# Kernel optimization log

Hardware: AMD Instinct MI355X
Metric: run time of the kernel (lower is better)

Reference implementation:

```python
import jax, jax.numpy as jnp
import numpy as np

B, S, H, L, V = 32, 128, 1024, 2, 32000


def setup_inputs() -> dict:
    key = jax.random.key(0)
    ks = jax.random.split(key, 9)
    scale = 1.0 / np.sqrt(H)
    return {
        "x": jax.random.randint(ks[0], (B, 1), 0, V),
        "hidden": jax.random.normal(ks[1], (L, B, H), jnp.float32) * 0.1,
        "cell": jax.random.normal(ks[2], (L, B, H), jnp.float32) * 0.1,
        "target": jax.random.randint(ks[3], (B, S), 0, V),
        "tf_ratio": 1,  # teacher forcing always on -> deterministic
        "emb": jax.random.normal(ks[4], (V, H), jnp.float32) * 0.02,
        "w_ih": jax.random.normal(ks[5], (L, 4 * H, H), jnp.float32) * scale,
        "w_hh": jax.random.normal(ks[6], (L, 4 * H, H), jnp.float32) * scale,
        "b_ih": jax.random.normal(ks[7], (L, 4 * H), jnp.float32) * scale,
        "b_hh": jax.random.normal(ks[8], (L, 4 * H), jnp.float32) * scale,
    }


def _lstm_decode(tokens, h0, c0, emb, w_ih, w_hh, b_ih, b_hh):
    # tokens: [B,S] int; embed all teacher-forced inputs at once
    x_seq = emb[tokens]                      # [B,S,H]
    x_tbh = jnp.swapaxes(x_seq, 0, 1)        # [S,B,H]
    n_layers = h0.shape[0]

    def step(carry, x_t):
        h, c = carry                         # each [L,B,H]
        inp = x_t                            # [B,H]
        hs, cs = [], []
        for l in range(n_layers):
            # PyTorch gate order: i, f, g, o
            z = inp @ w_ih[l].T + h[l] @ w_hh[l].T + b_ih[l] + b_hh[l]
            i, f, g, o = jnp.split(z, 4, axis=-1)
            c_new = jax.nn.sigmoid(f) * c[l] + jax.nn.sigmoid(i) * jnp.tanh(g)
            h_new = jax.nn.sigmoid(o) * jnp.tanh(c_new)
            hs.append(h_new)
            cs.append(c_new)
            inp = h_new
        return (jnp.stack(hs), jnp.stack(cs)), inp

    _, outs = jax.lax.scan(step, (h0, c0), x_tbh)  # outs: [S,B,H]
    out = jnp.swapaxes(outs, 0, 1)                 # [B,S,H]
    # tied-weight projection to vocab
    return jnp.einsum("bsh,vh->bsv", out, emb)     # [B,S,V]


def reference(x, hidden, cell, target, tf_ratio, emb, w_ih, w_hh, b_ih, b_hh):
    # tf_ratio == 1: step 0 consumes x, step i>=1 consumes target[:, i]
    tokens = jnp.concatenate([x, target[:, 1:]], axis=1)  # [B,S]
    return _lstm_decode(tokens, hidden, cell, emb, w_ih, w_hh, b_ih, b_hh)
```

## Files before the change

kernel.cpp:

```cpp
#include <hip/hip_runtime.h>
#include <stdint.h>


typedef __attribute__((ext_vector_type(8))) short short8;
typedef __attribute__((ext_vector_type(4))) float f32x4;

#define MFMA16(a, b, c) __builtin_amdgcn_mfma_f32_16x16x32_bf16((a), (b), (c), 0, 0, 0)

__device__ __forceinline__ unsigned short f2bf(float f) {
  union { float f; unsigned int u; } v; v.f = f;
  unsigned int u = v.u;
  return (unsigned short)((u + 0x7fffu + ((u >> 16) & 1u)) >> 16);
}

__device__ __forceinline__ void gload_lds16(const unsigned short* g, unsigned short* l) {
  __builtin_amdgcn_global_load_lds(
      (const __attribute__((address_space(1))) void*)g,
      (__attribute__((address_space(3))) void*)l, 16, 0, 0);
}

__device__ __forceinline__ void st_u32_dev(unsigned* p, unsigned v) {
  __hip_atomic_store(p, v, __ATOMIC_RELAXED, __HIP_MEMORY_SCOPE_AGENT);
}
__device__ __forceinline__ unsigned ld_u32_dev(const unsigned* p) {
  return __hip_atomic_load(p, __ATOMIC_RELAXED, __HIP_MEMORY_SCOPE_AGENT);
}


__global__ void cvt_bf16_k(const float* __restrict__ s, unsigned short* __restrict__ d, int n4) {
  int i = blockIdx.x * blockDim.x + threadIdx.x;
  int st = gridDim.x * blockDim.x;
  for (; i < n4; i += st) {
    float4 v = ((const float4*)s)[i];
    ushort4 o;
    o.x = f2bf(v.x); o.y = f2bf(v.y); o.z = f2bf(v.z); o.w = f2bf(v.w);
    ((ushort4*)d)[i] = o;
  }
}

__global__ void init_small_k(const float* __restrict__ hidden,
                             const float* __restrict__ b_ih, const float* __restrict__ b_hh,
                             unsigned short* __restrict__ h0, unsigned short* __restrict__ h1,
                             float* __restrict__ bsum) {
  int bb = blockIdx.x;
  int tid = threadIdx.x;
  if (bb < 64) {
    const float* src = hidden + (bb < 32 ? 0 : 32768);
    unsigned short* dst = (bb < 32) ? h0 : h1;
    int i = (bb & 31) * 256 + tid;
    float4 v = ((const float4*)src)[i];
    ushort4 u;
    u.x = f2bf(v.x); u.y = f2bf(v.y); u.z = f2bf(v.z); u.w = f2bf(v.w);
    ((ushort4*)dst)[i] = u;
  } else {
    int i = (bb - 64) * 256 + tid;
    bsum[i] = b_ih[i] + b_hh[i];
  }
}

__global__ void embed_k(const int* __restrict__ x, const int* __restrict__ tgt,
                        const float* __restrict__ emb, unsigned short* __restrict__ xseq) {
  int row = blockIdx.x;
  int t = row >> 5, b = row & 31;
  int tok = (t == 0) ? x[b] : tgt[b * 128 + t];
  const float4* e = (const float4*)(emb + (size_t)tok * 1024);
  ushort4* o = (ushort4*)(xseq + (size_t)row * 1024);
  int i = threadIdx.x;
  float4 v = e[i];
  ushort4 u;
  u.x = f2bf(v.x); u.y = f2bf(v.y); u.z = f2bf(v.z); u.w = f2bf(v.w);
  o[i] = u;
}


__global__ __launch_bounds__(256, 2) void gemm_bf16_k(
    const unsigned short* __restrict__ A, const unsigned short* __restrict__ B,
    float* __restrict__ C, const float* __restrict__ bias, int N, int permC) {
  __shared__ __align__(16) unsigned short smem[32768];
  const int tid = threadIdx.x;
  const int lane = tid & 63;
  const int w = tid >> 6;
  const int wm = w >> 1, wn = w & 1;
  const int xcd = blockIdx.x & 7;
  const int idx = blockIdx.x >> 3;
  const int nBase = (idx >> 2) * 128;
  const int mBase = (xcd * 4 + (idx & 3)) * 128;
  const int lr = lane & 15, lk = lane >> 4;
  const int K = 1024;

  const int srow = tid >> 3;
  const int scol = (tid & 7) ^ (srow & 7);
  const int wchunk = tid & 192;

  f32x4 acc[4][4];
#pragma unroll
  for (int i = 0; i < 4; ++i)
#pragma unroll
    for (int j = 0; j < 4; ++j) acc[i][j] = (f32x4){0.f, 0.f, 0.f, 0.f};

  const unsigned short* Ag = A + (size_t)mBase * K;
  const unsigned short* Bg = B + (size_t)nBase * K;

  auto stage = [&](int buf, int kt) {
    unsigned short* Ab = smem + buf * 16384;
    unsigned short* Bb = Ab + 8192;
#pragma unroll
    for (int r = 0; r < 4; ++r) {
      int row = r * 32 + srow;
      gload_lds16(Ag + (size_t)row * K + kt * 64 + scol * 8, &Ab[(r * 256 + wchunk) * 8]);
      gload_lds16(Bg + (size_t)row * K + kt * 64 + scol * 8, &Bb[(r * 256 + wchunk) * 8]);
    }
  };

  stage(0, 0);
  __syncthreads();
  for (int kt = 0; kt < 16; ++kt) {
    int cur = kt & 1;
    if (kt < 15) stage(cur ^ 1, kt + 1);
    const unsigned short* Ac = smem + cur * 16384;
    const unsigned short* Bc = Ac + 8192;
#pragma unroll
    for (int ks = 0; ks < 2; ++ks) {
      short8 a[4], b[4];
#pragma unroll
      for (int mf = 0; mf < 4; ++mf) {
        int row = wm * 64 + mf * 16 + lr;
        int cc = (ks * 4 + lk) ^ (row & 7);
        a[mf] = *(const short8*)&Ac[row * 64 + cc * 8];
      }
#pragma unroll
      for (int nf = 0; nf < 4; ++nf) {
        int row = wn * 64 + nf * 16 + lr;
        int cc = (ks * 4 + lk) ^ (row & 7);
        b[nf] = *(const short8*)&Bc[row * 64 + cc * 8];
      }
#pragma unroll
      for (int mf = 0; mf < 4; ++mf)
#pragma unroll
        for (int nf = 0; nf < 4; ++nf)
          acc[mf][nf] = MFMA16(a[mf], b[nf], acc[mf][nf]);
    }
    __syncthreads();
  }

  float* cst = (float*)smem;
#pragma unroll
  for (int r = 0; r < 4; ++r) {
    __syncthreads();
#pragma unroll
    for (int nf = 0; nf < 4; ++nf) {
      int col = wn * 64 + nf * 16 + lr;
      float bv = bias ? bias[nBase + col] : 0.f;
#pragma unroll
      for (int i = 0; i < 4; ++i)
        cst[(wm * 16 + lk * 4 + i) * 132 + col] = acc[r][nf][i] + bv;
    }
    __syncthreads();
#pragma unroll
    for (int pss = 0; pss < 4; ++pss) {
      int idxq = pss * 256 + tid;
      int rl = idxq >> 5, cq = idxq & 31;
      int ar = mBase + (rl >> 4) * 64 + r * 16 + (rl & 15);
      int cr = permC ? ((ar & 31) * 128 + (ar >> 5)) : ar;
      f32x4 v = *(const f32x4*)&cst[rl * 132 + cq * 4];
      __builtin_nontemporal_store(v, (f32x4*)&C[(size_t)cr * N + nBase + cq * 4]);
    }
  }
}


struct PParams {
  const float* zx0;
  const unsigned short* whh0;
  const unsigned short* wih1;
  const unsigned short* whh1;
  const float* bsum1;
  const float* cell;
  unsigned short* h0hist;
  const unsigned short* h1init;
  unsigned short* outb;
  unsigned int* slots0;
  unsigned int* slots1;
  unsigned int* queue;
  const unsigned short* embB;
  float* outC;
  int njobs;
};

__device__ __forceinline__ void proj_tile(int j, bool valid, int ltid, char* smbase,
                                          const unsigned short* Aout,
                                          const unsigned short* Bemb, float* C) {
  const int mB = j / 250, nB = j % 250;
  const int mBase = mB * 128, nBase = nB * 128;
  const int lane = ltid & 63;
  const int w4 = ltid >> 6;
  const int wm = w4 >> 1, wn = w4 & 1;
  const int lr = lane & 15, lk = lane >> 4;
  const int srow = ltid >> 3;
  const int scol = (ltid & 7) ^ (srow & 7);
  const int wchunk = ltid & 192;
  unsigned short* smem = (unsigned short*)smbase;

  f32x4 acc[4][4];
#pragma unroll
  for (int i = 0; i < 4; ++i)
#pragma unroll
    for (int q = 0; q < 4; ++q) acc[i][q] = (f32x4){0.f, 0.f, 0.f, 0.f};

  const unsigned short* Ag = Aout + (size_t)mBase * 1024;
  const unsigned short* Bg = Bemb + (size_t)nBase * 1024;

  auto stage = [&](int buf, int kt) {
    if (!valid) return;
    unsigned short* Ab = smem + buf * 16384;
    unsigned short* Bb = Ab + 8192;
#pragma unroll
    for (int r = 0; r < 4; ++r) {
      int row = r * 32 + srow;
      gload_lds16(Ag + (size_t)row * 1024 + kt * 64 + scol * 8, &Ab[(r * 256 + wchunk) * 8]);
      gload_lds16(Bg + (size_t)row * 1024 + kt * 64 + scol * 8, &Bb[(r * 256 + wchunk) * 8]);
    }
  };

  stage(0, 0);
  __syncthreads();
  for (int kt = 0; kt < 16; ++kt) {
    int cur = kt & 1;
    if (kt < 15) stage(cur ^ 1, kt + 1);
    const unsigned short* Ac = smem + cur * 16384;
    const unsigned short* Bc = Ac + 8192;
    if (valid) {
#pragma unroll
      for (int ks = 0; ks < 2; ++ks) {
        short8 a[4], b[4];
#pragma unroll
        for (int mf = 0; mf < 4; ++mf) {
          int row = wm * 64 + mf * 16 + lr;
          int cc = (ks * 4 + lk) ^ (row & 7);
          a[mf] = *(const short8*)&Ac[row * 64 + cc * 8];
        }
#pragma unroll
        for (int nf = 0; nf < 4; ++nf) {
          int row = wn * 64 + nf * 16 + lr;
          int cc = (ks * 4 + lk) ^ (row & 7);
          b[nf] = *(const short8*)&Bc[row * 64 + cc * 8];
        }
#pragma unroll
        for (int mf = 0; mf < 4; ++mf)
#pragma unroll
          for (int nf = 0; nf < 4; ++nf)
            acc[mf][nf] = MFMA16(a[mf], b[nf], acc[mf][nf]);
      }
    }
    __syncthreads();
  }

  float* cst = (float*)smem;
#pragma unroll
  for (int r = 0; r < 4; ++r) {
    __syncthreads();
    if (valid) {
#pragma unroll
      for (int nf = 0; nf < 4; ++nf) {
        int col = wn * 64 + nf * 16 + lr;
#pragma unroll
        for (int i = 0; i < 4; ++i)
          cst[(wm * 16 + lk * 4 + i) * 132 + col] = acc[r][nf][i];
      }
    }
    __syncthreads();
    if (valid) {
#pragma unroll
      for (int pss = 0; pss < 4; ++pss) {
        int idxq = pss * 256 + ltid;
        int rl = idxq >> 5, cq = idxq & 31;
        int ar = mBase + (rl >> 4) * 64 + r * 16 + (rl & 15);
        int cr = (ar & 31) * 128 + (ar >> 5);
        f32x4 v = *(const f32x4*)&cst[rl * 132 + cq * 4];
        __builtin_nontemporal_store(v, (f32x4*)&C[(size_t)cr * 32000 + nBase + cq * 4]);
      }
    }
  }
}

__global__ __launch_bounds__(512, 1) void lstm_persist_k(PParams P) {
  const int tid = threadIdx.x;
  const int lane = tid & 63;
  const int w = tid >> 6;
  const int lr = lane & 15, lkk = lane >> 4;

  __shared__ __align__(16) char pool[149504];
  __shared__ int jbase;
  unsigned short* wlds = (unsigned short*)pool;
  float* zraw = (float*)(pool + 131072);

  if (blockIdx.x < 64) {
    const int u0 = blockIdx.x * 16;
    const int m = w >> 2;
    const int gp = (w >> 1) & 1;
    const int kh = w & 1;
    const int g0 = gp * 2, g1 = gp * 2 + 1;

    for (int f = w; f < 128; f += 8) {
      int gg = f >> 5, kc = f & 31;
      const unsigned short* src =
          P.whh0 + (size_t)(gg * 1024 + u0 + lr) * 1024 + kc * 32 + lkk * 8;
      *(short8*)&wlds[f * 512 + lane * 8] = *(const short8*)src;
    }
    const int fb = tid >> 3;
    const int jp = tid & 7;
    float creg[2] = {0.f, 0.f};
    if (tid < 256) {
      creg[0] = P.cell[fb * 1024 + u0 + 2 * jp];
      creg[1] = P.cell[fb * 1024 + u0 + 2 * jp + 1];
    }
    __syncthreads();

    for (int i = 0; i < 128; ++i) {
      if (i > 0 && tid < 64) {
        const unsigned tgt = (unsigned)i;
        while (true) {
          unsigned v = ld_u32_dev(&P.slots0[tid * 32]);
          if (__all(v >= tgt)) break;
          __builtin_amdgcn_s_sleep(1);
        }
      }
      __syncthreads();

      float2 zr[4];
      if (tid < 256) {
        const float2* br = (const float2*)(P.zx0 + (size_t)i * 131072 + fb * 4096 + u0 + 2 * jp);
#pragma unroll
        for (int q = 0; q < 4; ++q) zr[q] = br[q * 512];
      }
      f32x4 acc0 = {0.f, 0.f, 0.f, 0.f}, acc1 = {0.f, 0.f, 0.f, 0.f};
      const unsigned short* ap =
          P.h0hist + (size_t)i * 32768 + (size_t)(m * 16 + lr) * 1024 + kh * 512 + lkk * 8;
#pragma unroll
      for (int g4 = 0; g4 < 2; ++g4) {
        short8 a[8];
#pragma unroll
        for (int q = 0; q < 8; ++q) a[q] = *(const short8*)(ap + (g4 * 8 + q) * 32);
#pragma unroll
        for (int q = 0; q < 8; ++q) {
          int kc = kh * 16 + g4 * 8 + q;
          short8 b0 = *(const short8*)&wlds[(g0 * 32 + kc) * 512 + lane * 8];
          short8 b1 = *(const short8*)&wlds[(g1 * 32 + kc) * 512 + lane * 8];
          acc0 = MFMA16(a[q], b0, acc0);
          acc1 = MFMA16(a[q], b1, acc1);
        }
      }
#pragma unroll
      for (int j = 0; j < 4; ++j) {
        zraw[(kh * 32 + m * 16 + lkk * 4 + j) * 72 + g0 * 16 + lr] = acc0[j];
        zraw[(kh * 32 + m * 16 + lkk * 4 + j) * 72 + g1 * 16 + lr] = acc1[j];
      }
      __syncthreads();

      if (tid < 256) {
        unsigned hv = 0;
#pragma unroll
        for (int u = 0; u < 2; ++u) {
          int j = 2 * jp + u;
          float zi = zraw[fb * 72 + j]      + zraw[(32 + fb) * 72 + j]      + ((u == 0) ? zr[0].x : zr[0].y);
          float zf = zraw[fb * 72 + 16 + j] + zraw[(32 + fb) * 72 + 16 + j] + ((u == 0) ? zr[1].x : zr[1].y);
          float zg = zraw[fb * 72 + 32 + j] + zraw[(32 + fb) * 72 + 32 + j] + ((u == 0) ? zr[2].x : zr[2].y);
          float zo = zraw[fb * 72 + 48 + j] + zraw[(32 + fb) * 72 + 48 + j] + ((u == 0) ? zr[3].x : zr[3].y);
          float ii = 1.f / (1.f + __expf(-zi));
          float ff = 1.f / (1.f + __expf(-zf));
          float gg = tanhf(zg);
          float oo = 1.f / (1.f + __expf(-zo));
          float cn = ff * creg[u] + ii * gg;
          creg[u] = cn;
          float hn = oo * tanhf(cn);
          hv |= ((unsigned)f2bf(hn)) << (16 * u);
        }
        st_u32_dev((unsigned*)&P.h0hist[(size_t)(i + 1) * 32768 + fb * 1024 + u0 + 2 * jp], hv);
      }
      __syncthreads();
      if (tid == 0) st_u32_dev(&P.slots0[blockIdx.x * 32], (unsigned)(i + 1));
    }
  } else if (blockIdx.x < 192) {
    const int u0 = (blockIdx.x - 64) * 8;
    const int slot = blockIdx.x - 64;
    const int mat = w >> 2;
    const int m = (w >> 1) & 1;
    const int kh = w & 1;

    for (int f = w; f < 128; f += 8) {
      int matf = f >> 6, nt = (f >> 5) & 1, kc = f & 31;
      int rr = nt * 16 + lr;
      int gate = rr >> 3, unit = rr & 7;
      const unsigned short* Wm = matf ? P.whh1 : P.wih1;
      const unsigned short* src =
          Wm + (size_t)(gate * 1024 + u0 + unit) * 1024 + kc * 32 + lkk * 8;
      *(short8*)&wlds[f * 512 + lane * 8] = *(const short8*)src;
    }
    const int fb = tid >> 2;
    const int jp = tid & 3;
    float creg[2] = {0.f, 0.f};
    float brg[4][2];
    if (tid < 128) {
      creg[0] = P.cell[32768 + fb * 1024 + u0 + 2 * jp];
      creg[1] = P.cell[32768 + fb * 1024 + u0 + 2 * jp + 1];
#pragma unroll
      for (int q = 0; q < 4; ++q) {
        brg[q][0] = P.bsum1[q * 1024 + u0 + 2 * jp];
        brg[q][1] = P.bsum1[q * 1024 + u0 + 2 * jp + 1];
      }
    }
    __syncthreads();

    for (int i = 1; i <= 128; ++i) {
      if (tid < 64) {
        const unsigned t0 = (unsigned)i, t1 = (unsigned)(i - 1);
        while (true) {
          bool ok = ld_u32_dev(&P.slots0[tid * 32]) >= t0;
          if (i > 1) {
            ok = ok && ld_u32_dev(&P.slots1[tid * 32]) >= t1
                    && ld_u32_dev(&P.slots1[(tid + 64) * 32]) >= t1;
          }
          if (__all(ok)) break;
          __builtin_amdgcn_s_sleep(2);
        }
      }
      __syncthreads();

      f32x4 acc0 = {0.f, 0.f, 0.f, 0.f}, acc1 = {0.f, 0.f, 0.f, 0.f};
      const unsigned short* ap;
      if (mat == 0) {
        ap = P.h0hist + (size_t)i * 32768 + (size_t)(m * 16 + lr) * 1024 + kh * 512 + lkk * 8;
      } else {
        const unsigned short* h1b =
            (i == 1) ? P.h1init : (P.outb + (size_t)(i - 2) * 32768);
        ap = h1b + (size_t)(m * 16 + lr) * 1024 + kh * 512 + lkk * 8;
      }
#pragma unroll
      for (int g4 = 0; g4 < 2; ++g4) {
        short8 a[8];
#pragma unroll
        for (int q = 0; q < 8; ++q) a[q] = *(const short8*)(ap + (g4 * 8 + q) * 32);
#pragma unroll
        for (int q = 0; q < 8; ++q) {
          int kc = kh * 16 + g4 * 8 + q;
          short8 b0 = *(const short8*)&wlds[(mat * 64 + 0 * 32 + kc) * 512 + lane * 8];
          short8 b1 = *(const short8*)&wlds[(mat * 64 + 1 * 32 + kc) * 512 + lane * 8];
          acc0 = MFMA16(a[q], b0, acc0);
          acc1 = MFMA16(a[q], b1, acc1);
        }
      }
      float* zp = zraw + (mat * 2 + kh) * 1152;
#pragma unroll
      for (int j = 0; j < 4; ++j) {
        zp[(m * 16 + lkk * 4 + j) * 36 + lr] = acc0[j];
        zp[(m * 16 + lkk * 4 + j) * 36 + 16 + lr] = acc1[j];
      }
      __syncthreads();

      if (tid < 128) {
        unsigned hv = 0;
#pragma unroll
        for (int u = 0; u < 2; ++u) {
          int j = 2 * jp + u;
          float z4[4];
#pragma unroll
          for (int q = 0; q < 4; ++q) {
            z4[q] = zraw[fb * 36 + q * 8 + j] + zraw[1152 + fb * 36 + q * 8 + j]
                  + zraw[2304 + fb * 36 + q * 8 + j] + zraw[3456 + fb * 36 + q * 8 + j]
                  + brg[q][u];
          }
          float ii = 1.f / (1.f + __expf(-z4[0]));
          float ff = 1.f / (1.f + __expf(-z4[1]));
          float gg = tanhf(z4[2]);
          float oo = 1.f / (1.f + __expf(-z4[3]));
          float cn = ff * creg[u] + ii * gg;
          creg[u] = cn;
          float hn = oo * tanhf(cn);
          hv |= ((unsigned)f2bf(hn)) << (16 * u);
        }
        st_u32_dev((unsigned*)&P.outb[(size_t)(i - 1) * 32768 + fb * 1024 + u0 + 2 * jp], hv);
      }
      __syncthreads();
      if (tid == 0) st_u32_dev(&P.slots1[slot * 32], (unsigned)i);
    }
  }

  while (true) {
    __syncthreads();
    if (tid == 0)
      jbase = (int)__hip_atomic_fetch_add(P.queue, 2u, __ATOMIC_RELAXED,
                                          __HIP_MEMORY_SCOPE_AGENT);
    __syncthreads();
    int base = jbase;
    if (base >= P.njobs) break;
    int j = base + (tid >> 8);
    bool valid = (j < P.njobs);
    int jmax = (base + 1 < P.njobs) ? base + 1 : base;
    int gateMB = jmax / 250;
    if (tid < 64) {
      unsigned tgt = (unsigned)(4 * gateMB + 4);
      if (tgt > 128u) tgt = 128u;
      while (true) {
        bool ok = ld_u32_dev(&P.slots1[tid * 32]) >= tgt &&
                  ld_u32_dev(&P.slots1[(tid + 64) * 32]) >= tgt;
        if (__all(ok)) break;
        __builtin_amdgcn_s_sleep(2);
      }
    }
    __syncthreads();
    proj_tile(j, valid, tid & 255, pool + (tid >> 8) * 65536, P.outb, P.embB, P.outC);
  }
}


extern "C" void kernel_launch(void* const* d_in, const int* in_sizes, int n_in,
                              void* d_out, int out_size, void* d_ws, size_t ws_size,
                              hipStream_t stream) {
  const int*   x      = (const int*)d_in[0];
  const float* hidden = (const float*)d_in[1];
  const float* cell   = (const float*)d_in[2];
  const int*   target = (const int*)d_in[3];
  const float* emb    = (const float*)d_in[5];
  const float* w_ih   = (const float*)d_in[6];
  const float* w_hh   = (const float*)d_in[7];
  const float* b_ih   = (const float*)d_in[8];
  const float* b_hh   = (const float*)d_in[9];
  float* out = (float*)d_out;
  char* ws = (char*)d_ws;

  unsigned short* emb_bf  = (unsigned short*)(ws);
  unsigned short* wih_bf  = (unsigned short*)(ws + 65536000);
  unsigned short* whh_bf  = (unsigned short*)(ws + 82313216);
  float*          bsum    = (float*)(ws + 99090432);
  unsigned short* outb    = (unsigned short*)(ws + 99123200);
  unsigned int*   barmem  = (unsigned int*)(ws + 107511808);
  unsigned short* h1init  = (unsigned short*)(ws + 107544576);

  const size_t WS_NEED = 107610112ull + 67108864ull + 8454144ull;
  const bool rich = (ws_size >= WS_NEED);
  float*          zx0    = rich ? (float*)(ws + 107610112)
                                : (float*)d_out;
  unsigned short* xseq   = rich ? (unsigned short*)d_out
                                : (unsigned short*)((char*)d_out + 67108864);
  unsigned short* h0hist = rich ? (unsigned short*)(ws + 174718976)
                                : (unsigned short*)((char*)d_out + 75497472);

  hipMemsetAsync(barmem, 0, 32768, stream);
  cvt_bf16_k<<<2048, 256, 0, stream>>>(emb, emb_bf, 8192000);
  cvt_bf16_k<<<2048, 256, 0, stream>>>(w_ih, wih_bf, 2097152);
  cvt_bf16_k<<<2048, 256, 0, stream>>>(w_hh, whh_bf, 2097152);
  init_small_k<<<96, 256, 0, stream>>>(hidden, b_ih, b_hh, h0hist, h1init, bsum);
  embed_k<<<4096, 256, 0, stream>>>(x, target, emb, xseq);

  gemm_bf16_k<<<1024, 256, 0, stream>>>(xseq, wih_bf, zx0, bsum, 4096, 0);

  PParams pp;
  pp.zx0 = zx0;
  pp.whh0 = whh_bf;
  pp.wih1 = wih_bf + 4194304;
  pp.whh1 = whh_bf + 4194304;
  pp.bsum1 = bsum + 4096;
  pp.cell = cell;
  pp.h0hist = h0hist;
  pp.h1init = h1init;
  pp.outb = outb;
  pp.slots0 = barmem;
  pp.slots1 = barmem + 2048;
  pp.queue = barmem + 6144;
  pp.embB = emb_bf;
  pp.outC = out;
  pp.njobs = rich ? 8000 : 0;
  lstm_persist_k<<<rich ? 256 : 192, 512, 0, stream>>>(pp);

  if (!rich) {
    gemm_bf16_k<<<8000, 256, 0, stream>>>(outb, emb_bf, out, nullptr, 32000, 1);
  }
}
```

Before: 1.083 ms.

## Distribute per-step flag polling across warps and prefetch all h operands before barrier

Each warp now polls only the producer slots covering its own K-half (and matrix) instead of one warp polling every slot and then releasing the whole block with a barrier. All 16 A-operand loads are issued right after the wait and before the block barrier, so global loads overlap the barrier and the MFMA loop runs without a mid-loop load group. This shortens the serial per-timestep critical path in the recurrent pipeline, at the cost of more registers for the 16-entry operand array and more concurrent polling traffic.

```diff
diff --git a/kernel.cpp b/kernel.cpp
--- a/kernel.cpp
+++ b/kernel.cpp
@@ -317,38 +317,32 @@
     __syncthreads();
 
     for (int i = 0; i < 128; ++i) {
-      if (i > 0 && tid < 64) {
-        const unsigned tgt = (unsigned)i;
-        while (true) {
-          unsigned v = ld_u32_dev(&P.slots0[tid * 32]);
-          if (__all(v >= tgt)) break;
-          __builtin_amdgcn_s_sleep(1);
-        }
-      }
-      __syncthreads();
-
       float2 zr[4];
       if (tid < 256) {
         const float2* br = (const float2*)(P.zx0 + (size_t)i * 131072 + fb * 4096 + u0 + 2 * jp);
 #pragma unroll
         for (int q = 0; q < 4; ++q) zr[q] = br[q * 512];
       }
-      f32x4 acc0 = {0.f, 0.f, 0.f, 0.f}, acc1 = {0.f, 0.f, 0.f, 0.f};
+      if (i > 0 && lane < 32) {
+        const unsigned tgt = (unsigned)i;
+        const unsigned* sl = &P.slots0[(kh * 32 + lane) * 32];
+        while (ld_u32_dev(sl) < tgt) __builtin_amdgcn_s_sleep(1);
+      }
+      short8 a[16];
       const unsigned short* ap =
           P.h0hist + (size_t)i * 32768 + (size_t)(m * 16 + lr) * 1024 + kh * 512 + lkk * 8;
 #pragma unroll
-      for (int g4 = 0; g4 < 2; ++g4) {
-        short8 a[8];
-#pragma unroll
-        for (int q = 0; q < 8; ++q) a[q] = *(const short8*)(ap + (g4 * 8 + q) * 32);
-#pragma unroll
-        for (int q = 0; q < 8; ++q) {
-          int kc = kh * 16 + g4 * 8 + q;
-          short8 b0 = *(const short8*)&wlds[(g0 * 32 + kc) * 512 + lane * 8];
-          short8 b1 = *(const short8*)&wlds[(g1 * 32 + kc) * 512 + lane * 8];
-          acc0 = MFMA16(a[q], b0, acc0);
-          acc1 = MFMA16(a[q], b1, acc1);
-        }
+      for (int q = 0; q < 16; ++q) a[q] = *(const short8*)(ap + q * 32);
+      __syncthreads();
+
+      f32x4 acc0 = {0.f, 0.f, 0.f, 0.f}, acc1 = {0.f, 0.f, 0.f, 0.f};
+#pragma unroll
+      for (int q = 0; q < 16; ++q) {
+        int kc = kh * 16 + q;
+        short8 b0 = *(const short8*)&wlds[(g0 * 32 + kc) * 512 + lane * 8];
+        short8 b1 = *(const short8*)&wlds[(g1 * 32 + kc) * 512 + lane * 8];
+        acc0 = MFMA16(a[q], b0, acc0);
+        acc1 = MFMA16(a[q], b1, acc1);
       }
 #pragma unroll
       for (int j = 0; j < 4; ++j) {
@@ -412,21 +406,18 @@
     __syncthreads();
 
     for (int i = 1; i <= 128; ++i) {
-      if (tid < 64) {
-        const unsigned t0 = (unsigned)i, t1 = (unsigned)(i - 1);
-        while (true) {
-          bool ok = ld_u32_dev(&P.slots0[tid * 32]) >= t0;
-          if (i > 1) {
-            ok = ok && ld_u32_dev(&P.slots1[tid * 32]) >= t1
-                    && ld_u32_dev(&P.slots1[(tid + 64) * 32]) >= t1;
-          }
-          if (__all(ok)) break;
-          __builtin_amdgcn_s_sleep(2);
+      if (mat == 0) {
+        if (lane < 32) {
+          const unsigned tgt = (unsigned)i;
+          const unsigned* sl = &P.slots0[(kh * 32 + lane) * 32];
+          while (ld_u32_dev(sl) < tgt) __builtin_amdgcn_s_sleep(2);
         }
-      }
-      __syncthreads();
-
-      f32x4 acc0 = {0.f, 0.f, 0.f, 0.f}, acc1 = {0.f, 0.f, 0.f, 0.f};
+      } else if (i > 1) {
+        const unsigned tgt = (unsigned)(i - 1);
+        const unsigned* sl = &P.slots1[(kh * 64 + lane) * 32];
+        while (ld_u32_dev(sl) < tgt) __builtin_amdgcn_s_sleep(2);
+      }
+      short8 a[16];
       const unsigned short* ap;
       if (mat == 0) {
         ap = P.h0hist + (size_t)i * 32768 + (size_t)(m * 16 + lr) * 1024 + kh * 512 + lkk * 8;
@@ -436,18 +427,17 @@
         ap = h1b + (size_t)(m * 16 + lr) * 1024 + kh * 512 + lkk * 8;
       }
 #pragma unroll
-      for (int g4 = 0; g4 < 2; ++g4) {
-        short8 a[8];
-#pragma unroll
-        for (int q = 0; q < 8; ++q) a[q] = *(const short8*)(ap + (g4 * 8 + q) * 32);
-#pragma unroll
-        for (int q = 0; q < 8; ++q) {
-          int kc = kh * 16 + g4 * 8 + q;
-          short8 b0 = *(const short8*)&wlds[(mat * 64 + 0 * 32 + kc) * 512 + lane * 8];
-          short8 b1 = *(const short8*)&wlds[(mat * 64 + 1 * 32 + kc) * 512 + lane * 8];
-          acc0 = MFMA16(a[q], b0, acc0);
-          acc1 = MFMA16(a[q], b1, acc1);
-        }
+      for (int q = 0; q < 16; ++q) a[q] = *(const short8*)(ap + q * 32);
+      __syncthreads();
+
+      f32x4 acc0 = {0.f, 0.f, 0.f, 0.f}, acc1 = {0.f, 0.f, 0.f, 0.f};
+#pragma unroll
+      for (int q = 0; q < 16; ++q) {
+        int kc = kh * 16 + q;
+        short8 b0 = *(const short8*)&wlds[(mat * 64 + 0 * 32 + kc) * 512 + lane * 8];
+        short8 b1 = *(const short8*)&wlds[(mat * 64 + 1 * 32 + kc) * 512 + lane * 8];
+        acc0 = MFMA16(a[q], b0, acc0);
+        acc1 = MFMA16(a[q], b1, acc1);
       }
       float* zp = zraw + (mat * 2 + kh) * 1152;
 #pragma unroll
```

After: 1.100 ms. Within noise of the previous version (+1.5%).
